# Kernel tuning notes

Hardware: AMD Instinct MI355X
Metric: run time of the kernel (lower is better)

## Reference

```python
import jax, jax.numpy as jnp
import numpy as np

B, S, D, H = 2, 2048, 2048, 16
DH = D // H


def setup_inputs() -> dict:
    key = jax.random.key(0)
    k1, k2, k3 = jax.random.split(key, 3)
    x = jax.random.normal(k1, (B, S, D), dtype=jnp.float32)
    Wqkv = jax.random.normal(k2, (D, 3 * D), dtype=jnp.float32) * (1.0 / np.sqrt(D))
    bqkv = jnp.zeros((3 * D,), dtype=jnp.float32)
    Wproj = jax.random.normal(k3, (D, D), dtype=jnp.float32) * (1.0 / np.sqrt(D))
    bproj = jnp.zeros((D,), dtype=jnp.float32)
    return {"x": x, "Wqkv": Wqkv, "bqkv": bqkv, "Wproj": Wproj, "bproj": bproj}


def reference(x, Wqkv, bqkv, Wproj, bproj):
    b, s, d = x.shape
    h, dh = H, DH
    # fused qkv projection: [b, s, 3, h, dh]
    qkv = (x @ Wqkv + bqkv).reshape(b, s, 3, h, dh)
    q, k, v = qkv[:, :, 0], qkv[:, :, 1], qkv[:, :, 2]  # each [b, s, h, dh]
    scale = 1.0 / np.sqrt(dh).astype(np.float32)
    # scores [b, h, q, k]
    attn = jnp.einsum('bqhd,bkhd->bhqk', q, k) * scale
    causal = jnp.tril(jnp.ones((s, s), dtype=bool))  # [s, s]
    attn = jnp.where(causal[None, None], attn, -jnp.inf)
    attn = jax.nn.softmax(attn, axis=-1)
    out = jnp.einsum('bhqk,bkhd->bqhd', attn, v).reshape(b, s, d)
    return out @ Wproj + bproj
```

## Files before the change

### kernel.cpp

```cpp
#include <hip/hip_runtime.h>
#include <hip/hip_bf16.h>

#define BB 2
#define SS 2048
#define DD 2048
#define HH 16
#define DHH 128
#define MM 4096
#define NN1 6144
#define NTILES (DD / 64)

typedef __attribute__((ext_vector_type(8))) short bf16x8;
typedef __attribute__((ext_vector_type(4))) float f32x4;
typedef unsigned int u32;

static __device__ __forceinline__ float exp2_hw(float x) {
  return __builtin_amdgcn_exp2f(x);
}

static __device__ __forceinline__ unsigned short f2bf(float f) {
  union { float f; u32 u; } v; v.f = f;
  return (unsigned short)((v.u + 0x7FFFu + ((v.u >> 16) & 1u)) >> 16);
}

static __device__ __forceinline__ void gload_lds16(const void* g, void* l) {
  __builtin_amdgcn_global_load_lds((const __attribute__((address_space(1))) u32*)g,
                                   (__attribute__((address_space(3))) u32*)l, 16, 0, 0);
}

__global__ __launch_bounds__(256) void k_cvt(const float* __restrict__ in,
                                             unsigned short* __restrict__ out) {
  int i = blockIdx.x * 256 + threadIdx.x;
  float4 v = ((const float4*)in)[i];
  ushort4 o;
  o.x = f2bf(v.x); o.y = f2bf(v.y); o.z = f2bf(v.z); o.w = f2bf(v.w);
  ((ushort4*)out)[i] = o;
}

__global__ __launch_bounds__(256) void k_transpose(const float* __restrict__ in,
                                                   unsigned short* __restrict__ out,
                                                   int R, int C) {
  __shared__ float t[32][33];
  int bx = blockIdx.x * 32, by = blockIdx.y * 32;
  int tx = threadIdx.x, ty = threadIdx.y;
  #pragma unroll
  for (int i = ty; i < 32; i += 8)
    t[i][tx] = in[(size_t)(by + i) * C + bx + tx];
  __syncthreads();
  #pragma unroll
  for (int i = ty; i < 32; i += 8)
    out[(size_t)(bx + i) * R + by + tx] = f2bf(t[tx][i]);
}

__device__ __forceinline__ void gemm_core(const char* __restrict__ Ag,
                                          const char* __restrict__ Bg,
                                          char* Alds, char* Blds,
                                          f32x4 acc[4][4]) {
  const int tid = threadIdx.x;
  const int wave = tid >> 6, lane = tid & 63;
  const int g = lane >> 4, c = lane & 15;
  const int wm = wave >> 1, wn = wave & 1;

  auto stageA = [&](int buf, int kt) {
    #pragma unroll
    for (int q = 0; q < 4; ++q) {
      int off = q * 8192 + wave * 1024 + (lane << 4);
      int row = off >> 7, cb = off & 127;
      gload_lds16(Ag + (size_t)row * 4096 + kt * 128 + (cb ^ ((row & 7) << 4)),
                  Alds + buf * 32768 + q * 8192 + wave * 1024);
    }
  };
  auto stageB = [&](int buf, int kt) {
    #pragma unroll
    for (int q = 0; q < 2; ++q) {
      int off = q * 8192 + wave * 1024 + (lane << 4);
      int row = off >> 7, cb = off & 127;
      gload_lds16(Bg + (size_t)row * 4096 + kt * 128 + (cb ^ ((row & 7) << 4)),
                  Blds + buf * 16384 + q * 8192 + wave * 1024);
    }
  };

  stageA(0, 0); stageB(0, 0);
  stageA(1, 1); stageB(1, 1);
  asm volatile("s_waitcnt vmcnt(6)" ::: "memory");
  __builtin_amdgcn_sched_barrier(0);
  __builtin_amdgcn_s_barrier();

  for (int t = 0; t < NTILES; ++t) {
    const int buf = t % 3;
    const char* Ab = Alds + buf * 32768;
    const char* Bb = Blds + buf * 16384;
    bf16x8 af[4][2], bfv[4][2];
    #pragma unroll
    for (int i = 0; i < 4; ++i) {
      int row = wm * 64 + i * 16 + c;
      af[i][0] = *(const bf16x8*)(Ab + row * 128 + ((g * 16) ^ ((row & 7) << 4)));
    }
    #pragma unroll
    for (int j = 0; j < 4; ++j) {
      int row = wn * 64 + j * 16 + c;
      bfv[j][0] = *(const bf16x8*)(Bb + row * 128 + ((g * 16) ^ ((row & 7) << 4)));
    }
    __builtin_amdgcn_sched_barrier(0);
    #pragma unroll
    for (int i = 0; i < 4; ++i) {
      int row = wm * 64 + i * 16 + c;
      af[i][1] = *(const bf16x8*)(Ab + row * 128 + ((64 + g * 16) ^ ((row & 7) << 4)));
    }
    #pragma unroll
    for (int j = 0; j < 4; ++j) {
      int row = wn * 64 + j * 16 + c;
      bfv[j][1] = *(const bf16x8*)(Bb + row * 128 + ((64 + g * 16) ^ ((row & 7) << 4)));
    }
    if (t + 2 < NTILES) {
      int nb = buf + 2; if (nb >= 3) nb -= 3;
      stageA(nb, t + 2);
      stageB(nb, t + 2);
    }
    asm volatile("s_waitcnt lgkmcnt(8)" ::: "memory");
    __builtin_amdgcn_sched_barrier(0);
    __builtin_amdgcn_s_setprio(1);
    #pragma unroll
    for (int i = 0; i < 4; ++i)
      #pragma unroll
      for (int j = 0; j < 4; ++j)
        acc[i][j] = __builtin_amdgcn_mfma_f32_16x16x32_bf16(af[i][0], bfv[j][0], acc[i][j], 0, 0, 0);
    __builtin_amdgcn_s_setprio(0);
    asm volatile("s_waitcnt lgkmcnt(0)" ::: "memory");
    __builtin_amdgcn_sched_barrier(0);
    __builtin_amdgcn_s_setprio(1);
    #pragma unroll
    for (int i = 0; i < 4; ++i)
      #pragma unroll
      for (int j = 0; j < 4; ++j)
        acc[i][j] = __builtin_amdgcn_mfma_f32_16x16x32_bf16(af[i][1], bfv[j][1], acc[i][j], 0, 0, 0);
    __builtin_amdgcn_s_setprio(0);
    if (t < NTILES - 1) {
      if (t + 2 < NTILES) { asm volatile("s_waitcnt vmcnt(6)" ::: "memory"); }
      else                { asm volatile("s_waitcnt vmcnt(0)" ::: "memory"); }
      __builtin_amdgcn_sched_barrier(0);
      __builtin_amdgcn_s_barrier();
    }
  }
}

__global__ __launch_bounds__(512, 1) void k_gemm1(const unsigned short* __restrict__ A,
                                                  const unsigned short* __restrict__ Bt,
                                                  const float* __restrict__ bias,
                                                  unsigned short* __restrict__ Qb,
                                                  unsigned short* __restrict__ Kb,
                                                  unsigned short* __restrict__ Vt) {
  __shared__ __align__(16) char lds[147456];
  const int n0 = blockIdx.x * 128, m0 = blockIdx.y * 256;
  f32x4 acc[4][4] = {};
  gemm_core((const char*)A + (size_t)m0 * 4096,
            (const char*)Bt + (size_t)n0 * 4096,
            lds, lds + 98304, acc);
  const int lane = threadIdx.x & 63, wave = threadIdx.x >> 6;
  const int g = lane >> 4, c = lane & 15;
  const int wm = wave >> 1, wn = wave & 1;
  const int head = (n0 >> 7) & 15, which = n0 >> 11;
  const float qsc = 0.12751879523263566f;
  #pragma unroll
  for (int i = 0; i < 4; ++i) {
    int rowb = m0 + wm * 64 + i * 16 + g * 4;
    int bb = rowb >> 11, s = rowb & 2047;
    #pragma unroll
    for (int j = 0; j < 4; ++j) {
      int dh = wn * 64 + j * 16 + c;
      float bv = bias[n0 + dh];
      if (which == 2) {
        ushort4 p;
        p.x = f2bf(acc[i][j][0] + bv);
        p.y = f2bf(acc[i][j][1] + bv);
        p.z = f2bf(acc[i][j][2] + bv);
        p.w = f2bf(acc[i][j][3] + bv);
        *(ushort4*)(Vt + ((size_t)(bb * HH + head) * DHH + dh) * SS + s) = p;
      } else {
        float v0 = acc[i][j][0] + bv, v1 = acc[i][j][1] + bv;
        float v2 = acc[i][j][2] + bv, v3 = acc[i][j][3] + bv;
        if (which == 0) { v0 *= qsc; v1 *= qsc; v2 *= qsc; v3 *= qsc; }
        unsigned short* dst = (which == 0 ? Qb : Kb) + ((size_t)(bb * HH + head) * SS + s) * DHH + dh;
        dst[0]       = f2bf(v0);
        dst[DHH]     = f2bf(v1);
        dst[2 * DHH] = f2bf(v2);
        dst[3 * DHH] = f2bf(v3);
      }
    }
  }
}

__global__ __launch_bounds__(512, 1) void k_gemm2(const unsigned short* __restrict__ A,
                                                  const unsigned short* __restrict__ Bt,
                                                  const float* __restrict__ bias,
                                                  float* __restrict__ out) {
  __shared__ __align__(16) char lds[147456];
  const int n0 = blockIdx.x * 128, m0 = blockIdx.y * 256;
  f32x4 acc[4][4] = {};
  gemm_core((const char*)A + (size_t)m0 * 4096,
            (const char*)Bt + (size_t)n0 * 4096,
            lds, lds + 98304, acc);
  const int lane = threadIdx.x & 63, wave = threadIdx.x >> 6;
  const int g = lane >> 4, c = lane & 15;
  const int wm = wave >> 1, wn = wave & 1;
  #pragma unroll
  for (int i = 0; i < 4; ++i) {
    int rowb = m0 + wm * 64 + i * 16 + g * 4;
    #pragma unroll
    for (int j = 0; j < 4; ++j) {
      int gcol = n0 + wn * 64 + j * 16 + c;
      float bv = bias[gcol];
      #pragma unroll
      for (int r = 0; r < 4; ++r)
        out[(size_t)(rowb + r) * DD + gcol] = acc[i][j][r] + bv;
    }
  }
}

__global__ __launch_bounds__(256, 2) void k_attn(const unsigned short* __restrict__ Qb,
                                                 const unsigned short* __restrict__ Kb,
                                                 const unsigned short* __restrict__ Vt,
                                                 unsigned short* __restrict__ O) {
  __shared__ __align__(16) unsigned short Kt[2][64 * 128];
  __shared__ __align__(16) unsigned short Vs[2][128 * 64];
  __shared__ __align__(16) unsigned short Pl[4][32 * 64];
  const int qtl = (blockIdx.y < 16) ? blockIdx.x : (15 - blockIdx.x);
  const int bh = blockIdx.y;
  const int b = bh >> 4, h = bh & 15;
  const int tid = threadIdx.x, wave = tid >> 6, lane = tid & 63;
  const int g = lane >> 4, c = lane & 15;
  const int q0w = qtl * 128 + wave * 32;
  const unsigned short* Qp = Qb + (size_t)bh * SS * DHH;
  const unsigned short* Kp = Kb + (size_t)bh * SS * DHH;
  const unsigned short* Vp = Vt + (size_t)bh * DHH * SS;

  bf16x8 qf[2][4];
  #pragma unroll
  for (int m = 0; m < 2; ++m)
    #pragma unroll
    for (int ks = 0; ks < 4; ++ks)
      qf[m][ks] = *(const bf16x8*)(Qp + (size_t)(q0w + m * 16 + c) * DHH + ks * 32 + g * 8);

  f32x4 acc[2][8] = {};
  float mrow[2] = {-1e30f, -1e30f}, lsum[2] = {0.f, 0.f};

  auto stage = [&](int buf, int kv0) {
    #pragma unroll
    for (int r = 0; r < 4; ++r) {
      int base = r * 4096 + wave * 1024;
      int off = base + (lane << 4);
      { int row = off >> 8; int cb = (off & 255) ^ ((row & 7) << 4);
        gload_lds16((const char*)Kp + (size_t)(kv0 + row) * 256 + cb,
                    (char*)Kt[buf] + base); }
      { int row = off >> 7; int cb = (off & 127) ^ ((row & 7) << 4);
        gload_lds16((const char*)Vp + (size_t)row * (SS * 2) + (size_t)kv0 * 2 + cb,
                    (char*)Vs[buf] + base); }
    }
  };

  const int ntiles = 2 * qtl + 2;
  stage(0, 0);
  __syncthreads();

  for (int t = 0; t < ntiles; ++t) {
    const int cur = t & 1;
    const int kv0 = t * 64;
    if (t + 1 < ntiles) stage(cur ^ 1, kv0 + 64);
    if (kv0 <= q0w + 31) {
      const unsigned short* K_ = Kt[cur];
      const unsigned short* V_ = Vs[cur];
      f32x4 sa[2][4] = {};
      __builtin_amdgcn_s_setprio(1);
      #pragma unroll
      for (int nb = 0; nb < 4; ++nb) {
        const int rk = nb * 16 + c;
        const int swz = (rk & 7) << 4;
        #pragma unroll
        for (int ks = 0; ks < 4; ++ks) {
          bf16x8 kf = *(const bf16x8*)((const char*)K_ + rk * 256 + ((ks * 64 + g * 16) ^ swz));
          sa[0][nb] = __builtin_amdgcn_mfma_f32_16x16x32_bf16(kf, qf[0][ks], sa[0][nb], 0, 0, 0);
          sa[1][nb] = __builtin_amdgcn_mfma_f32_16x16x32_bf16(kf, qf[1][ks], sa[1][nb], 0, 0, 0);
        }
      }
      __builtin_amdgcn_s_setprio(0);
      #pragma unroll
      for (int m = 0; m < 2; ++m) {
        const int q = q0w + m * 16 + c;
        float p[4][4];
        float tm = -1e30f;
        #pragma unroll
        for (int nb = 0; nb < 4; ++nb)
          #pragma unroll
          for (int r = 0; r < 4; ++r) {
            float s = sa[m][nb][r];
            if (kv0 + nb * 16 + g * 4 + r > q) s = -1e30f;
            p[nb][r] = s;
            tm = fmaxf(tm, s);
          }
        tm = fmaxf(tm, __shfl_xor(tm, 16, 64));
        tm = fmaxf(tm, __shfl_xor(tm, 32, 64));
        float mr = mrow[m];
        if (__any(tm > mr + 11.0f)) {
          float mnew = fmaxf(mr, tm);
          float sf = exp2_hw(mr - mnew);
          lsum[m] *= sf;
          float sfr[4];
          #pragma unroll
          for (int r = 0; r < 4; ++r)
            sfr[r] = __shfl(sf, 20 * g + r, 64);
          #pragma unroll
          for (int nf = 0; nf < 8; ++nf)
            #pragma unroll
            for (int r = 0; r < 4; ++r) acc[m][nf][r] *= sfr[r];
          mrow[m] = mnew; mr = mnew;
        }
        float rs = 0.f;
        #pragma unroll
        for (int nb = 0; nb < 4; ++nb)
          #pragma unroll
          for (int r = 0; r < 4; ++r) {
            p[nb][r] = exp2_hw(p[nb][r] - mr);
            rs += p[nb][r];
          }
        rs += __shfl_xor(rs, 16, 64);
        rs += __shfl_xor(rs, 32, 64);
        lsum[m] += rs;
        const int rowp = m * 16 + c;
        const int swzp = (rowp & 7) << 4;
        #pragma unroll
        for (int nb = 0; nb < 4; ++nb)
          #pragma unroll
          for (int i2 = 0; i2 < 2; ++i2) {
            u32 w = (u32)f2bf(p[nb][2 * i2]) | ((u32)f2bf(p[nb][2 * i2 + 1]) << 16);
            *(u32*)((char*)Pl[wave] + rowp * 128 + (((nb * 16 + g * 4 + 2 * i2) * 2) ^ swzp)) = w;
          }
      }
      asm volatile("s_waitcnt lgkmcnt(0)" ::: "memory");
      __builtin_amdgcn_sched_barrier(0);
      bf16x8 pf[2][2];
      #pragma unroll
      for (int m = 0; m < 2; ++m)
        #pragma unroll
        for (int c2 = 0; c2 < 2; ++c2) {
          int rowp = m * 16 + c;
          pf[m][c2] = *(const bf16x8*)((const char*)Pl[wave] + rowp * 128 +
                                       ((c2 * 64 + g * 16) ^ ((rowp & 7) << 4)));
        }
      __builtin_amdgcn_s_setprio(1);
      #pragma unroll
      for (int nf = 0; nf < 8; ++nf) {
        const int rv = nf * 16 + c;
        const int swzv = (rv & 7) << 4;
        #pragma unroll
        for (int c2 = 0; c2 < 2; ++c2) {
          bf16x8 vf = *(const bf16x8*)((const char*)V_ + rv * 128 + ((c2 * 64 + g * 16) ^ swzv));
          acc[0][nf] = __builtin_amdgcn_mfma_f32_16x16x32_bf16(pf[0][c2], vf, acc[0][nf], 0, 0, 0);
          acc[1][nf] = __builtin_amdgcn_mfma_f32_16x16x32_bf16(pf[1][c2], vf, acc[1][nf], 0, 0, 0);
        }
      }
      __builtin_amdgcn_s_setprio(0);
    }
    __syncthreads();
  }

  unsigned short* Op = O + (size_t)b * SS * DD + (size_t)h * DHH;
  #pragma unroll
  for (int m = 0; m < 2; ++m) {
    float inv = 1.0f / lsum[m];
    float invr[4];
    #pragma unroll
    for (int r = 0; r < 4; ++r)
      invr[r] = __shfl(inv, 20 * g + r, 64);
    #pragma unroll
    for (int nf = 0; nf < 8; ++nf)
      #pragma unroll
      for (int r = 0; r < 4; ++r) {
        int q = q0w + m * 16 + g * 4 + r;
        Op[(size_t)q * DD + nf * 16 + c] = f2bf(acc[m][nf][r] * invr[r]);
      }
  }
}

extern "C" void kernel_launch(void* const* d_in, const int* in_sizes, int n_in,
                              void* d_out, int out_size, void* d_ws, size_t ws_size,
                              hipStream_t stream) {
  const float* x     = (const float*)d_in[0];
  const float* Wqkv  = (const float*)d_in[1];
  const float* bqkv  = (const float*)d_in[2];
  const float* Wproj = (const float*)d_in[3];
  const float* bproj = (const float*)d_in[4];
  float* out = (float*)d_out;

  char* ws = (char*)d_ws;
  unsigned short* xb  = (unsigned short*)ws; ws += (size_t)MM * DD * 2;
  unsigned short* w1t = (unsigned short*)ws; ws += (size_t)NN1 * DD * 2;
  unsigned short* w2t = (unsigned short*)ws; ws += (size_t)DD * DD * 2;
  unsigned short* Qb  = (unsigned short*)ws; ws += (size_t)BB * HH * SS * DHH * 2;
  unsigned short* Kb  = (unsigned short*)ws; ws += (size_t)BB * HH * SS * DHH * 2;
  unsigned short* Vt  = (unsigned short*)ws; ws += (size_t)BB * HH * SS * DHH * 2;
  unsigned short* Ob  = (unsigned short*)ws; ws += (size_t)MM * DD * 2;

  k_cvt<<<dim3((MM * DD) / 1024), 256, 0, stream>>>(x, xb);
  k_transpose<<<dim3(NN1 / 32, DD / 32), dim3(32, 8), 0, stream>>>(Wqkv, w1t, DD, NN1);
  k_transpose<<<dim3(DD / 32, DD / 32), dim3(32, 8), 0, stream>>>(Wproj, w2t, DD, DD);
  k_gemm1<<<dim3(NN1 / 128, MM / 256), 512, 0, stream>>>(xb, w1t, bqkv, Qb, Kb, Vt);
  k_attn<<<dim3(SS / 128, BB * HH), 256, 0, stream>>>(Qb, Kb, Vt, Ob);
  k_gemm2<<<dim3(DD / 128, MM / 256), 512, 0, stream>>>(Ob, w2t, bproj, out);
}
```

Baseline: 265.4 us.

## Use BK=32 triple-buffered GEMM core in QKV projection for two blocks per CU

Adds a new GEMM main loop with a K-tile of 32 and three LDS buffers in place of the previous 64-wide tile. QKV GEMM LDS use drops from 144 KB to 72 KB, and launch bounds now request two blocks per CU. The goal is to raise occupancy so one block's latency can be hidden by another. In exchange there are twice as many barriers per K step and fewer MFMAs between syncs, and register pressure may limit the second block.

```diff
diff --git a/kernel.cpp b/kernel.cpp
--- a/kernel.cpp
+++ b/kernel.cpp
@@ -9,6 +9,7 @@
 #define MM 4096
 #define NN1 6144
 #define NTILES (DD / 64)
+#define NT32 (DD / 32)
 
 typedef __attribute__((ext_vector_type(8))) short bf16x8;
 typedef __attribute__((ext_vector_type(4))) float f32x4;
@@ -50,6 +51,75 @@
   #pragma unroll
   for (int i = ty; i < 32; i += 8)
     out[(size_t)(bx + i) * R + by + tx] = f2bf(t[tx][i]);
+}
+
+__device__ __forceinline__ void gemm_core_bk32(const char* __restrict__ Ag,
+                                               const char* __restrict__ Bg,
+                                               char* lds, f32x4 acc[4][4]) {
+  const int tid = threadIdx.x;
+  const int wave = tid >> 6, lane = tid & 63;
+  const int g = lane >> 4, c = lane & 15;
+  const int wm = wave >> 1, wn = wave & 1;
+
+  auto stage = [&](int buf, int kt) {
+    char* base = lds + buf * 24576;
+    #pragma unroll
+    for (int q = 0; q < 2; ++q) {
+      int off = q * 8192 + tid * 16;
+      int row = off >> 6, cb = off & 63;
+      gload_lds16(Ag + (size_t)row * 4096 + kt * 64 + (cb ^ (((row >> 1) & 3) << 4)),
+                  base + q * 8192 + wave * 1024);
+    }
+    {
+      int off = tid * 16;
+      int row = off >> 6, cb = off & 63;
+      gload_lds16(Bg + (size_t)row * 4096 + kt * 64 + (cb ^ (((row >> 1) & 3) << 4)),
+                  base + 16384 + wave * 1024);
+    }
+  };
+
+  stage(0, 0);
+  stage(1, 1);
+  asm volatile("s_waitcnt vmcnt(3)" ::: "memory");
+  __builtin_amdgcn_sched_barrier(0);
+  __builtin_amdgcn_s_barrier();
+
+  int buf = 0;
+  for (int t = 0; t < NT32; ++t) {
+    if (t + 2 < NT32) {
+      int nb = buf + 2; if (nb >= 3) nb -= 3;
+      stage(nb, t + 2);
+    }
+    const char* Ab = lds + buf * 24576;
+    const char* Bb = Ab + 16384;
+    bf16x8 af[4], bfv[4];
+    #pragma unroll
+    for (int i = 0; i < 4; ++i) {
+      int row = wm * 64 + i * 16 + c;
+      af[i] = *(const bf16x8*)(Ab + row * 64 + ((g * 16) ^ (((row >> 1) & 3) << 4)));
+    }
+    #pragma unroll
+    for (int j = 0; j < 4; ++j) {
+      int row = wn * 64 + j * 16 + c;
+      bfv[j] = *(const bf16x8*)(Bb + row * 64 + ((g * 16) ^ (((row >> 1) & 3) << 4)));
+    }
+    asm volatile("s_waitcnt lgkmcnt(0)" ::: "memory");
+    __builtin_amdgcn_sched_barrier(0);
+    __builtin_amdgcn_s_setprio(1);
+    #pragma unroll
+    for (int i = 0; i < 4; ++i)
+      #pragma unroll
+      for (int j = 0; j < 4; ++j)
+        acc[i][j] = __builtin_amdgcn_mfma_f32_16x16x32_bf16(af[i], bfv[j], acc[i][j], 0, 0, 0);
+    __builtin_amdgcn_s_setprio(0);
+    if (t < NT32 - 1) {
+      if (t + 2 < NT32) { asm volatile("s_waitcnt vmcnt(3)" ::: "memory"); }
+      else              { asm volatile("s_waitcnt vmcnt(0)" ::: "memory"); }
+      __builtin_amdgcn_sched_barrier(0);
+      __builtin_amdgcn_s_barrier();
+    }
+    ++buf; if (buf == 3) buf = 0;
+  }
 }
 
 __device__ __forceinline__ void gemm_core(const char* __restrict__ Ag,
@@ -144,18 +214,18 @@
   }
 }
 
-__global__ __launch_bounds__(512, 1) void k_gemm1(const unsigned short* __restrict__ A,
+__global__ __launch_bounds__(512, 2) void k_gemm1(const unsigned short* __restrict__ A,
                                                   const unsigned short* __restrict__ Bt,
                                                   const float* __restrict__ bias,
                                                   unsigned short* __restrict__ Qb,
                                                   unsigned short* __restrict__ Kb,
                                                   unsigned short* __restrict__ Vt) {
-  __shared__ __align__(16) char lds[147456];
+  __shared__ __align__(16) char lds[73728];
   const int n0 = blockIdx.x * 128, m0 = blockIdx.y * 256;
   f32x4 acc[4][4] = {};
-  gemm_core((const char*)A + (size_t)m0 * 4096,
-            (const char*)Bt + (size_t)n0 * 4096,
-            lds, lds + 98304, acc);
+  gemm_core_bk32((const char*)A + (size_t)m0 * 4096,
+                 (const char*)Bt + (size_t)n0 * 4096,
+                 lds, acc);
   const int lane = threadIdx.x & 63, wave = threadIdx.x >> 6;
   const int g = lane >> 4, c = lane & 15;
   const int wm = wave >> 1, wn = wave & 1;
```

Result: no change. 265.8 us (+0.1%).
